# Kernel optimization log

Measured on AMD Instinct MI355X. Metric: run time of the kernel, lower is better.

Reference implementation:

```python
import jax, jax.numpy as jnp
import numpy as np

H, Dh = 8, 64          # heads, per-head dim
FEA = H * Dh           # 512
B, T, N = 2, 128, 128
BETA = 0.3
EPS = 1e-5
SEG = T // H


def _ln(x):
    # LayerNorm over last dim, no affine params (elementwise_affine=False)
    m = jnp.mean(x, axis=-1, keepdims=True)
    v = jnp.mean((x - m) ** 2, axis=-1, keepdims=True)
    return (x - m) / jnp.sqrt(v + EPS)


def setup_inputs() -> dict:
    key = jax.random.key(0)
    ks = jax.random.split(key, 10)
    mkw = lambda k: jax.random.normal(k, (FEA, FEA), jnp.float32) * 0.02
    return {
        "x": jax.random.normal(ks[0], (B, T, N, FEA), jnp.float32),
        "te": jax.random.normal(ks[1], (B, T, N, FEA), jnp.float32),
        "Wq": mkw(ks[2]), "bq": jnp.zeros((FEA,), jnp.float32),
        "Wk": mkw(ks[3]), "bk": jnp.zeros((FEA,), jnp.float32),
        "Wv": mkw(ks[4]), "bv": jnp.zeros((FEA,), jnp.float32),
        "Wo": mkw(ks[5]), "bo": jnp.zeros((FEA,), jnp.float32),
        "W1": mkw(ks[6]), "b1": jnp.zeros((FEA,), jnp.float32),
        "W2": mkw(ks[7]), "b2": jnp.zeros((FEA,), jnp.float32),
    }


def reference(x, te, Wq, bq, Wk, bk, Wv, bv, Wo, bo, W1, b1, W2, b2):
    xt = x + te                                        # [B,T,N,F]
    q = (xt @ Wq + bq).reshape(B, T, N, H, Dh)
    k = (xt @ Wk + bk).reshape(B, T, N, H, Dh)
    v = (xt @ Wv + bv).reshape(B, T, N, H, Dh)

    # scores[b,h,n,s,t] = q_s . k_t / sqrt(d)
    scores = jnp.einsum('bsnhd,btnhd->bhnst', q, k) / np.sqrt(Dh).astype(np.float32)

    # causal mask (Mask=True): key t <= query s
    causal = jnp.tril(jnp.ones((T, T), dtype=bool))
    scores = jnp.where(causal[None, None, None], scores, -jnp.inf)

    # segment-focus reweighting (Mask2=True): head i keeps key columns
    # [i*SEG, (i+1)*SEG) (last head extends to T) at full weight, scales
    # everything else by BETA. (-inf * BETA stays -inf.)
    cols = jnp.arange(T)
    start = jnp.arange(H) * SEG
    end = jnp.where(jnp.arange(H) == H - 1, T, start + SEG)
    focus = (cols[None, :] >= start[:, None]) & (cols[None, :] < end[:, None])  # [H,T]
    scores = jnp.where(focus[None, :, None, None, :], scores, scores * BETA)

    attn = jax.nn.softmax(scores, axis=-1)
    out = jnp.einsum('bhnst,btnhd->bsnhd', attn, v).reshape(B, T, N, FEA)

    out = out @ Wo + bo
    out = _ln(out + xt)

    # FeedForward([F,F,F], res_ln=True): linear-relu-linear + residual + LN
    h = jax.nn.relu(out @ W1 + b1)
    h = h @ W2 + b2
    return _ln(h + out)
```

## Files before the change

### kernel.cpp

```cpp
#include <hip/hip_runtime.h>
#include <math.h>

typedef unsigned int uint;
typedef unsigned short ushort;

#define FEA 512
#define NH 8
#define DH 64
#define BB 2
#define TT 128
#define NN 128
#define MTOT (BB*TT*NN)
#define SEG 16
#define BETA 0.3f
#define LNEPS 1e-5f

typedef __attribute__((ext_vector_type(8))) _Float16 f16x8;
typedef __attribute__((ext_vector_type(4))) float f32x4;
typedef __attribute__((ext_vector_type(8))) short s16x8;

static __device__ __forceinline__ ushort f2h(float x) {
  _Float16 h = (_Float16)x;
  return __builtin_bit_cast(ushort, h);
}
static __device__ __forceinline__ float h2f(ushort u) {
  return (float)__builtin_bit_cast(_Float16, u);
}

__global__ __launch_bounds__(256) void add_h(const float* __restrict__ x,
                                             const float* __restrict__ te,
                                             ushort* __restrict__ xth) {
  size_t i = ((size_t)blockIdx.x * 256 + threadIdx.x) * 8;
  float4 a0 = *(const float4*)&x[i];
  float4 a1 = *(const float4*)&x[i + 4];
  float4 b0 = *(const float4*)&te[i];
  float4 b1 = *(const float4*)&te[i + 4];
  s16x8 o;
  o[0]=(short)f2h(a0.x+b0.x); o[1]=(short)f2h(a0.y+b0.y);
  o[2]=(short)f2h(a0.z+b0.z); o[3]=(short)f2h(a0.w+b0.w);
  o[4]=(short)f2h(a1.x+b1.x); o[5]=(short)f2h(a1.y+b1.y);
  o[6]=(short)f2h(a1.z+b1.z); o[7]=(short)f2h(a1.w+b1.w);
  *(s16x8*)&xth[i] = o;
}

struct W6 { const float* s[6]; };

__global__ __launch_bounds__(256) void wconv(W6 w, ushort* __restrict__ dst) {
  __shared__ float t[32][33];
  const float* W = w.s[blockIdx.z];
  ushort* WT = dst + (size_t)blockIdx.z * FEA * FEA;
  const int k0 = blockIdx.y * 32, n0 = blockIdx.x * 32;
  const int tx = threadIdx.x & 31, ty = threadIdx.x >> 5;
  #pragma unroll
  for (int i = 0; i < 4; ++i)
    t[ty + i * 8][tx] = W[(size_t)(k0 + ty + i * 8) * FEA + n0 + tx];
  __syncthreads();
  #pragma unroll
  for (int i = 0; i < 4; ++i)
    WT[(size_t)(n0 + ty + i * 8) * FEA + k0 + tx] = f2h(t[tx][ty + i * 8]);
}

template<int RELU>
__global__ __launch_bounds__(256) void gemm_h(const ushort* __restrict__ A,
                                              const ushort* __restrict__ WT,
                                              const float* __restrict__ bias,
                                              ushort* __restrict__ C) {
  __shared__ ushort As[128 * 32];
  __shared__ ushort Bs[128 * 32];
  const int tid = threadIdx.x;
  const int m0 = blockIdx.y * 128;
  const int n0 = blockIdx.x * 128;
  const int lane = tid & 63;
  const int wid = tid >> 6;
  const int wm = wid >> 1, wn = wid & 1;
  const int c = lane & 15, g = lane >> 4;

  f32x4 acc[4][4] = {};

  int r_[2], kq_[2];
  #pragma unroll
  for (int cc = 0; cc < 2; ++cc) {
    int i = cc * 256 + tid;
    r_[cc] = i >> 2;
    kq_[cc] = (i & 3) ^ ((r_[cc] >> 1) & 3);
  }

  for (int k0 = 0; k0 < 512; k0 += 32) {
    #pragma unroll
    for (int cc = 0; cc < 2; ++cc) {
      const ushort* ga = A  + (size_t)(m0 + r_[cc]) * 512 + k0 + kq_[cc] * 8;
      const ushort* gb = WT + (size_t)(n0 + r_[cc]) * 512 + k0 + kq_[cc] * 8;
      __builtin_amdgcn_global_load_lds(
          (const __attribute__((address_space(1))) void*)ga,
          (__attribute__((address_space(3))) void*)&As[(cc * 256 + tid) * 8], 16, 0, 0);
      __builtin_amdgcn_global_load_lds(
          (const __attribute__((address_space(1))) void*)gb,
          (__attribute__((address_space(3))) void*)&Bs[(cc * 256 + tid) * 8], 16, 0, 0);
    }
    __syncthreads();

    f16x8 af[4], bfr[4];
    #pragma unroll
    for (int s = 0; s < 4; ++s) {
      int ra = wm * 64 + s * 16 + c;
      int sa = ra * 4 + (g ^ ((ra >> 1) & 3));
      af[s] = *(const f16x8*)&As[sa * 8];
      int rb = wn * 64 + s * 16 + c;
      int sb = rb * 4 + (g ^ ((rb >> 1) & 3));
      bfr[s] = *(const f16x8*)&Bs[sb * 8];
    }
    #pragma unroll
    for (int i = 0; i < 4; ++i)
      #pragma unroll
      for (int j = 0; j < 4; ++j)
        acc[i][j] = __builtin_amdgcn_mfma_f32_16x16x32_f16(bfr[j], af[i], acc[i][j], 0, 0, 0);
    __syncthreads();
  }

  float4 bv4[4];
  #pragma unroll
  for (int j = 0; j < 4; ++j)
    bv4[j] = *(const float4*)&bias[n0 + wn * 64 + j * 16 + g * 4];
  #pragma unroll
  for (int i = 0; i < 4; ++i) {
    const size_t rb = (size_t)(m0 + wm * 64 + i * 16 + c) * 512;
    #pragma unroll
    for (int j = 0; j < 4; ++j) {
      const int nb = n0 + wn * 64 + j * 16 + g * 4;
      float o0 = acc[i][j][0] + bv4[j].x;
      float o1 = acc[i][j][1] + bv4[j].y;
      float o2 = acc[i][j][2] + bv4[j].z;
      float o3 = acc[i][j][3] + bv4[j].w;
      if (RELU) {
        o0 = fmaxf(o0, 0.f); o1 = fmaxf(o1, 0.f);
        o2 = fmaxf(o2, 0.f); o3 = fmaxf(o3, 0.f);
      }
      uint2 pk;
      pk.x = (uint)f2h(o0) | ((uint)f2h(o1) << 16);
      pk.y = (uint)f2h(o2) | ((uint)f2h(o3) << 16);
      *(uint2*)&C[rb + nb] = pk;
    }
  }
}

__global__ __launch_bounds__(256) void attn_mfma(const ushort* __restrict__ kp,
                                                 const ushort* __restrict__ vp,
                                                 ushort* __restrict__ qo) {
  __shared__ ushort Ks[8192];
  __shared__ ushort Vt[8192];
  __shared__ ushort Pb[4][1024];
  __shared__ float  Lb[4][32];

  const int bid = blockIdx.x;
  const int h = bid & 7;
  const int n = (bid >> 3) & 127;
  const int b = bid >> 10;
  const int tid = threadIdx.x;
  const int lane = tid & 63;
  const int w = tid >> 6;
  const int g = lane >> 4, c = lane & 15;
  const size_t tstride = (size_t)NN * FEA;
  const size_t base = ((size_t)b * TT * NN + n) * FEA + (size_t)h * DH;

  #pragma unroll
  for (int it = 0; it < 4; ++it) {
    int i = it * 256 + tid;
    int t = i >> 3;
    int gd = (i & 7) ^ (t & 7);
    const ushort* gk = kp + base + (size_t)t * tstride + gd * 8;
    __builtin_amdgcn_global_load_lds(
        (const __attribute__((address_space(1))) void*)gk,
        (__attribute__((address_space(3))) void*)&Ks[i * 8], 16, 0, 0);
  }
  #pragma unroll
  for (int it = 0; it < 4; ++it) {
    int j = it * 256 + tid;
    int t = j >> 3, d0 = (j & 7) * 8;
    s16x8 vv = *(const s16x8*)&vp[base + (size_t)t * tstride + d0];
    #pragma unroll
    for (int jj = 0; jj < 8; ++jj) {
      int d = d0 + jj;
      int slot = d * 16 + ((t >> 3) ^ (d & 7) ^ (d >> 3));
      Vt[slot * 8 + (t & 7)] = (ushort)vv[jj];
    }
  }
  const int qb = w * 32;
  f16x8 Qf[2][2];
  #pragma unroll
  for (int qt = 0; qt < 2; ++qt)
    #pragma unroll
    for (int kf = 0; kf < 2; ++kf)
      Qf[qt][kf] = *(const f16x8*)
          &qo[base + (size_t)(qb + qt * 16 + c) * tstride + kf * 32 + g * 8];
  __syncthreads();

  const int fs = h * SEG;
  const int fe = (h == NH - 1) ? TT : fs + SEG;

  f32x4 Oa[2][4];
  #pragma unroll
  for (int qt = 0; qt < 2; ++qt)
    #pragma unroll
    for (int dt = 0; dt < 4; ++dt)
      Oa[qt][dt] = (f32x4){0.f, 0.f, 0.f, 0.f};
  float lsum[2] = {0.f, 0.f};

  for (int ch = 0; ch <= w; ++ch) {
    const int tc = ch * 32;
    f32x4 sf[2][2];
    #pragma unroll
    for (int tt2 = 0; tt2 < 2; ++tt2) {
      f16x8 Kf[2];
      #pragma unroll
      for (int kf = 0; kf < 2; ++kf) {
        int t = tc + tt2 * 16 + c;
        int slot = t * 8 + ((kf * 4 + g) ^ (c & 7));
        Kf[kf] = *(const f16x8*)&Ks[slot * 8];
      }
      #pragma unroll
      for (int qt = 0; qt < 2; ++qt) {
        f32x4 s = (f32x4){0.f, 0.f, 0.f, 0.f};
        s = __builtin_amdgcn_mfma_f32_16x16x32_f16(Kf[0], Qf[qt][0], s, 0, 0, 0);
        s = __builtin_amdgcn_mfma_f32_16x16x32_f16(Kf[1], Qf[qt][1], s, 0, 0, 0);
        sf[tt2][qt] = s;
      }
    }
    #pragma unroll
    for (int tt2 = 0; tt2 < 2; ++tt2) {
      #pragma unroll
      for (int qt = 0; qt < 2; ++qt) {
        const int q = qb + qt * 16 + c;
        const int qr = qt * 16 + c;
        #pragma unroll
        for (int pr = 0; pr < 2; ++pr) {
          float pv[2];
          #pragma unroll
          for (int rr = 0; rr < 2; ++rr) {
            int reg = pr * 2 + rr;
            int t = tc + tt2 * 16 + g * 4 + reg;
            float mult = (t >= fs && t < fe) ? 0.125f : 0.125f * BETA;
            float p = __expf(sf[tt2][qt][reg] * mult);
            p = (t <= q) ? p : 0.f;
            pv[rr] = p;
            lsum[qt] += p;
          }
          uint pk = (uint)f2h(pv[0]) | ((uint)f2h(pv[1]) << 16);
          int tl = tt2 * 16 + g * 4 + pr * 2;
          int slot = qr * 4 + ((tl >> 3) ^ (qr & 3));
          *(uint*)&Pb[w][slot * 8 + (tl & 7)] = pk;
        }
      }
    }
    f16x8 Vf[4];
    #pragma unroll
    for (int dt = 0; dt < 4; ++dt) {
      int d = dt * 16 + c;
      int slot = d * 16 + ((((tc >> 3)) + g) ^ (d & 7) ^ (d >> 3));
      Vf[dt] = *(const f16x8*)&Vt[slot * 8];
    }
    #pragma unroll
    for (int qt = 0; qt < 2; ++qt) {
      int qr = qt * 16 + c;
      int slot = qr * 4 + (g ^ (qr & 3));
      f16x8 Pa = *(const f16x8*)&Pb[w][slot * 8];
      #pragma unroll
      for (int dt = 0; dt < 4; ++dt)
        Oa[qt][dt] = __builtin_amdgcn_mfma_f32_16x16x32_f16(Pa, Vf[dt], Oa[qt][dt], 0, 0, 0);
    }
  }

  #pragma unroll
  for (int qt = 0; qt < 2; ++qt) {
    lsum[qt] += __shfl_xor(lsum[qt], 16, 64);
    lsum[qt] += __shfl_xor(lsum[qt], 32, 64);
  }
  if (g == 0) {
    Lb[w][c]      = 1.0f / lsum[0];
    Lb[w][16 + c] = 1.0f / lsum[1];
  }
  #pragma unroll
  for (int qt = 0; qt < 2; ++qt) {
    f32x4 linv = *(const f32x4*)&Lb[w][qt * 16 + g * 4];
    #pragma unroll
    for (int dt = 0; dt < 4; ++dt) {
      #pragma unroll
      for (int reg = 0; reg < 4; ++reg) {
        int q = qb + qt * 16 + g * 4 + reg;
        qo[base + (size_t)q * tstride + dt * 16 + c] = f2h(Oa[qt][dt][reg] * linv[reg]);
      }
    }
  }
}

template<int AH, int RH, int OH>
__global__ __launch_bounds__(256) void ln_add(const void* __restrict__ a_,
                                              const void* __restrict__ r_,
                                              void* __restrict__ y_) {
  const int lane = threadIdx.x & 63;
  const int w = threadIdx.x >> 6;
  const size_t row = (size_t)blockIdx.x * 4 + w;
  const size_t off = row * FEA + (size_t)lane * 8;
  float ua[8], ur[8], u[8];
  if (AH) {
    s16x8 v = *(const s16x8*)&((const ushort*)a_)[off];
    #pragma unroll
    for (int j = 0; j < 8; ++j) ua[j] = h2f((ushort)v[j]);
  } else {
    float4 v0 = *(const float4*)&((const float*)a_)[off];
    float4 v1 = *(const float4*)&((const float*)a_)[off + 4];
    ua[0]=v0.x; ua[1]=v0.y; ua[2]=v0.z; ua[3]=v0.w;
    ua[4]=v1.x; ua[5]=v1.y; ua[6]=v1.z; ua[7]=v1.w;
  }
  if (RH) {
    s16x8 v = *(const s16x8*)&((const ushort*)r_)[off];
    #pragma unroll
    for (int j = 0; j < 8; ++j) ur[j] = h2f((ushort)v[j]);
  } else {
    float4 v0 = *(const float4*)&((const float*)r_)[off];
    float4 v1 = *(const float4*)&((const float*)r_)[off + 4];
    ur[0]=v0.x; ur[1]=v0.y; ur[2]=v0.z; ur[3]=v0.w;
    ur[4]=v1.x; ur[5]=v1.y; ur[6]=v1.z; ur[7]=v1.w;
  }
  float sum = 0.f, sq = 0.f;
  #pragma unroll
  for (int j = 0; j < 8; ++j) {
    u[j] = ua[j] + ur[j];
    sum += u[j];
    sq = fmaf(u[j], u[j], sq);
  }
  #pragma unroll
  for (int m = 1; m < 64; m <<= 1) {
    sum += __shfl_xor(sum, m, 64);
    sq  += __shfl_xor(sq,  m, 64);
  }
  const float mean = sum * (1.0f / FEA);
  const float var = sq * (1.0f / FEA) - mean * mean;
  const float rstd = rsqrtf(var + LNEPS);
  if (OH) {
    s16x8 o;
    #pragma unroll
    for (int j = 0; j < 8; ++j) o[j] = (short)f2h((u[j] - mean) * rstd);
    *(s16x8*)&((ushort*)y_)[off] = o;
  } else {
    float4 o0, o1;
    o0.x=(u[0]-mean)*rstd; o0.y=(u[1]-mean)*rstd; o0.z=(u[2]-mean)*rstd; o0.w=(u[3]-mean)*rstd;
    o1.x=(u[4]-mean)*rstd; o1.y=(u[5]-mean)*rstd; o1.z=(u[6]-mean)*rstd; o1.w=(u[7]-mean)*rstd;
    *(float4*)&((float*)y_)[off] = o0;
    *(float4*)&((float*)y_)[off + 4] = o1;
  }
}

extern "C" void kernel_launch(void* const* d_in, const int* in_sizes, int n_in,
                              void* d_out, int out_size, void* d_ws, size_t ws_size,
                              hipStream_t stream) {
  const float* x  = (const float*)d_in[0];
  const float* te = (const float*)d_in[1];
  const float* bq = (const float*)d_in[3];
  const float* bk = (const float*)d_in[5];
  const float* bv = (const float*)d_in[7];
  const float* bo = (const float*)d_in[9];
  const float* b1 = (const float*)d_in[11];
  const float* b2 = (const float*)d_in[13];
  float* out = (float*)d_out;

  const size_t E = (size_t)MTOT * FEA;
  ushort* B0 = (ushort*)d_ws;
  ushort* B1 = B0 + E;
  ushort* B2 = B1 + E;
  ushort* B3 = B2 + E;
  ushort* WB = B3 + E;
  const size_t WE = (size_t)FEA * FEA;

  dim3 gGemm(4, 256);

  add_h<<<E / 8 / 256, 256, 0, stream>>>(x, te, B0);
  W6 w;
  w.s[0] = (const float*)d_in[2];  w.s[1] = (const float*)d_in[4];
  w.s[2] = (const float*)d_in[6];  w.s[3] = (const float*)d_in[8];
  w.s[4] = (const float*)d_in[10]; w.s[5] = (const float*)d_in[12];
  wconv<<<dim3(16, 16, 6), 256, 0, stream>>>(w, WB);
  gemm_h<0><<<gGemm, 256, 0, stream>>>(B0, WB + 0 * WE, bq, B1);
  gemm_h<0><<<gGemm, 256, 0, stream>>>(B0, WB + 1 * WE, bk, B2);
  gemm_h<0><<<gGemm, 256, 0, stream>>>(B0, WB + 2 * WE, bv, B3);
  attn_mfma<<<BB * NN * NH, 256, 0, stream>>>(B2, B3, B1);
  gemm_h<0><<<gGemm, 256, 0, stream>>>(B1, WB + 3 * WE, bo, B2);
  ln_add<1, 1, 1><<<MTOT / 4, 256, 0, stream>>>(B2, B0, B0);
  gemm_h<1><<<gGemm, 256, 0, stream>>>(B0, WB + 4 * WE, b1, B3);
  gemm_h<0><<<gGemm, 256, 0, stream>>>(B3, WB + 5 * WE, b2, B1);
  ln_add<1, 1, 0><<<MTOT / 4, 256, 0, stream>>>(B1, B0, out);
}
```

Before: 454.2 us.

## Double-buffer GEMM LDS tiles and fuse Q/K/V projections into one launch

The GEMM kernel now uses two LDS buffers, issuing the next k-tile's global-to-LDS loads before computing on the current one, so load latency can overlap the MFMA work. The three Q/K/V projection GEMMs are merged into a single launch with a 12-wide grid, where each block selects its weight, bias and output from a small argument struct. This removes two kernel launches and gives a larger grid per launch, at the cost of doubled LDS use (32KB per block), which may lower occupancy. There is only one barrier per iteration, so the prefetch into the other buffer relies on the previous iteration's trailing barrier to avoid overwriting data still being read.

Result: no change. 450.1 us (-0.9%).

```diff
diff --git a/kernel.cpp b/kernel.cpp
--- a/kernel.cpp
+++ b/kernel.cpp
@@ -60,16 +60,23 @@
     WT[(size_t)(n0 + ty + i * 8) * FEA + k0 + tx] = f2h(t[tx][ty + i * 8]);
 }
 
-template<int RELU>
-__global__ __launch_bounds__(256) void gemm_h(const ushort* __restrict__ A,
-                                              const ushort* __restrict__ WT,
-                                              const float* __restrict__ bias,
-                                              ushort* __restrict__ C) {
-  __shared__ ushort As[128 * 32];
-  __shared__ ushort Bs[128 * 32];
+struct GArgs {
+  const ushort* wt[3];
+  const float* bias[3];
+  ushort* out[3];
+};
+
+template<int RELU, int NW>
+__global__ __launch_bounds__(256) void gemm_h(const ushort* __restrict__ A, GArgs p) {
+  __shared__ ushort As[2][4096];
+  __shared__ ushort Bs[2][4096];
   const int tid = threadIdx.x;
   const int m0 = blockIdx.y * 128;
-  const int n0 = blockIdx.x * 128;
+  const int wsel = (NW == 3) ? (blockIdx.x >> 2) : 0;
+  const int n0 = ((NW == 3) ? (blockIdx.x & 3) : blockIdx.x) * 128;
+  const ushort* __restrict__ WT = p.wt[wsel];
+  const float*  __restrict__ bias = p.bias[wsel];
+  ushort* __restrict__ C = p.out[wsel];
   const int lane = tid & 63;
   const int wid = tid >> 6;
   const int wm = wid >> 1, wn = wid & 1;
@@ -85,36 +92,44 @@
     kq_[cc] = (i & 3) ^ ((r_[cc] >> 1) & 3);
   }
 
-  for (int k0 = 0; k0 < 512; k0 += 32) {
+  auto stage = [&](int buf, int k0) {
     #pragma unroll
     for (int cc = 0; cc < 2; ++cc) {
       const ushort* ga = A  + (size_t)(m0 + r_[cc]) * 512 + k0 + kq_[cc] * 8;
       const ushort* gb = WT + (size_t)(n0 + r_[cc]) * 512 + k0 + kq_[cc] * 8;
       __builtin_amdgcn_global_load_lds(
           (const __attribute__((address_space(1))) void*)ga,
-          (__attribute__((address_space(3))) void*)&As[(cc * 256 + tid) * 8], 16, 0, 0);
+          (__attribute__((address_space(3))) void*)&As[buf][(cc * 256 + tid) * 8], 16, 0, 0);
       __builtin_amdgcn_global_load_lds(
           (const __attribute__((address_space(1))) void*)gb,
-          (__attribute__((address_space(3))) void*)&Bs[(cc * 256 + tid) * 8], 16, 0, 0);
-    }
-    __syncthreads();
+          (__attribute__((address_space(3))) void*)&Bs[buf][(cc * 256 + tid) * 8], 16, 0, 0);
+    }
+  };
+
+  stage(0, 0);
+  __syncthreads();
+  int cur = 0;
+  for (int t = 0; t < 16; ++t) {
+    if (t < 15) stage(cur ^ 1, (t + 1) * 32);
 
     f16x8 af[4], bfr[4];
     #pragma unroll
     for (int s = 0; s < 4; ++s) {
       int ra = wm * 64 + s * 16 + c;
       int sa = ra * 4 + (g ^ ((ra >> 1) & 3));
-      af[s] = *(const f16x8*)&As[sa * 8];
+      af[s] = *(const f16x8*)&As[cur][sa * 8];
       int rb = wn * 64 + s * 16 + c;
       int sb = rb * 4 + (g ^ ((rb >> 1) & 3));
-      bfr[s] = *(const f16x8*)&Bs[sb * 8];
+      bfr[s] = *(const f16x8*)&Bs[cur][sb * 8];
     }
     #pragma unroll
     for (int i = 0; i < 4; ++i)
       #pragma unroll
       for (int j = 0; j < 4; ++j)
         acc[i][j] = __builtin_amdgcn_mfma_f32_16x16x32_f16(bfr[j], af[i], acc[i][j], 0, 0, 0);
+
     __syncthreads();
+    cur ^= 1;
   }
 
   float4 bv4[4];
@@ -371,21 +386,27 @@
   ushort* WB = B3 + E;
   const size_t WE = (size_t)FEA * FEA;
 
-  dim3 gGemm(4, 256);
-
   add_h<<<E / 8 / 256, 256, 0, stream>>>(x, te, B0);
   W6 w;
   w.s[0] = (const float*)d_in[2];  w.s[1] = (const float*)d_in[4];
   w.s[2] = (const float*)d_in[6];  w.s[3] = (const float*)d_in[8];
   w.s[4] = (const float*)d_in[10]; w.s[5] = (const float*)d_in[12];
   wconv<<<dim3(16, 16, 6), 256, 0, stream>>>(w, WB);
-  gemm_h<0><<<gGemm, 256, 0, stream>>>(B0, WB + 0 * WE, bq, B1);
-  gemm_h<0><<<gGemm, 256, 0, stream>>>(B0, WB + 1 * WE, bk, B2);
-  gemm_h<0><<<gGemm, 256, 0, stream>>>(B0, WB + 2 * WE, bv, B3);
+  GArgs gqkv;
+  gqkv.wt[0] = WB;          gqkv.bias[0] = bq; gqkv.out[0] = B1;
+  gqkv.wt[1] = WB + WE;     gqkv.bias[1] = bk; gqkv.out[1] = B2;
+  gqkv.wt[2] = WB + 2 * WE; gqkv.bias[2] = bv; gqkv.out[2] = B3;
+  gemm_h<0, 3><<<dim3(12, 256), 256, 0, stream>>>(B0, gqkv);
   attn_mfma<<<BB * NN * NH, 256, 0, stream>>>(B2, B3, B1);
-  gemm_h<0><<<gGemm, 256, 0, stream>>>(B1, WB + 3 * WE, bo, B2);
+  GArgs go = {};
+  go.wt[0] = WB + 3 * WE; go.bias[0] = bo; go.out[0] = B2;
+  gemm_h<0, 1><<<dim3(4, 256), 256, 0, stream>>>(B1, go);
   ln_add<1, 1, 1><<<MTOT / 4, 256, 0, stream>>>(B2, B0, B0);
-  gemm_h<1><<<gGemm, 256, 0, stream>>>(B0, WB + 4 * WE, b1, B3);
-  gemm_h<0><<<gGemm, 256, 0, stream>>>(B3, WB + 5 * WE, b2, B1);
+  GArgs g1 = {};
+  g1.wt[0] = WB + 4 * WE; g1.bias[0] = b1; g1.out[0] = B3;
+  gemm_h<1, 1><<<dim3(4, 256), 256, 0, stream>>>(B0, g1);
+  GArgs g2 = {};
+  g2.wt[0] = WB + 5 * WE; g2.bias[0] = b2; g2.out[0] = B1;
+  gemm_h<0, 1><<<dim3(4, 256), 256, 0, stream>>>(B3, g2);
   ln_add<1, 1, 0><<<MTOT / 4, 256, 0, stream>>>(B1, B0, out);
 }
```
